# Optimization experiments

Hardware: AMD Instinct MI355X
Metric: run time of the kernel (lower is better)

## Reference

```python
import jax, jax.numpy as jnp
import numpy as np

B, T, C, H = 2, 2048, 1024, 16
D = C // H
EPS = 1e-5
ROPE_BASE = 10000.0


def _rope_tables(t, d, base=ROPE_BASE):
    half = d // 2
    inv_freq = 1.0 / (base ** (jnp.arange(half, dtype=jnp.float32) / half))
    freqs = jnp.arange(t, dtype=jnp.float32)[:, None] * inv_freq[None, :]  # [T, D/2]
    emb = jnp.concatenate([freqs, freqs], axis=-1)  # [T, D]
    return jnp.cos(emb), jnp.sin(emb)


def _rotate_half(x):
    a, b = jnp.split(x, 2, axis=-1)
    return jnp.concatenate([-b, a], axis=-1)


def setup_inputs() -> dict:
    key = jax.random.key(0)
    k0, k1, k2 = jax.random.split(key, 3)
    s = 0.02  # typical init scale
    return {
        "x": jax.random.normal(k0, (B, T, C), jnp.float32),
        "attention_mask": jnp.ones((B, T), jnp.int32),
        "w_qkv": jax.random.normal(k1, (3 * C, C), jnp.float32) * s,
        "b_qkv": jnp.zeros((3 * C,), jnp.float32),
        "w_o": jax.random.normal(k2, (C, C), jnp.float32) * s,
        "b_o": jnp.zeros((C,), jnp.float32),
        "rms_w": jnp.ones((C,), jnp.float32),
    }


def reference(x, attention_mask, w_qkv, b_qkv, w_o, b_o, rms_w):
    b, t, c = x.shape
    h = H
    d = c // h
    # RMSNorm
    xn = x * jax.lax.rsqrt(jnp.mean(x * x, axis=-1, keepdims=True) + EPS) * rms_w
    # fused QKV projection -> [B, T, 3, H, D]
    qkv = (jnp.einsum('btc,oc->bto', xn, w_qkv) + b_qkv).reshape(b, t, 3, h, d)
    q, k, v = qkv[:, :, 0], qkv[:, :, 1], qkv[:, :, 2]
    # RoPE (position_ids = arange(T))
    cos, sin = _rope_tables(t, d)
    cos = cos[None, :, None, :]  # [1, T, 1, D]
    sin = sin[None, :, None, :]
    q = q * cos + _rotate_half(q) * sin
    k = k * cos + _rotate_half(k) * sin
    # causal attention (flash_attn_func semantics: scale 1/sqrt(d), causal)
    scores = jnp.einsum('bqhd,bkhd->bhqk', q, k) / jnp.sqrt(jnp.float32(d))
    causal = jnp.tril(jnp.ones((t, t), dtype=bool))
    scores = jnp.where(causal[None, None], scores, jnp.float32(-1e30))
    attn = jax.nn.softmax(scores, axis=-1)
    out = jnp.einsum('bhqk,bkhd->bqhd', attn, v).reshape(b, t, c)
    return jnp.einsum('btc,oc->bto', out, w_o) + b_o
```

## Files before the change

kernel.cpp:

```cpp
#include <hip/hip_runtime.h>
#include <math.h>

constexpr int Bb = 2;
constexpr int Tt = 2048;
constexpr int Cc = 1024;
constexpr int Hh = 16;
constexpr int M_ROWS = Bb * Tt;
constexpr float EPSV = 1e-5f;

typedef __attribute__((ext_vector_type(4))) float f32x4;
typedef __attribute__((ext_vector_type(8))) __bf16 bf16x8;
using u16 = unsigned short;

union Frag8 {
    u16 u[8];
    unsigned int ui[4];
    uint4 v;
    bf16x8 b;
};

__device__ __forceinline__ u16 f2bf(float f) {
    union { float f; unsigned int u; } c;
    c.f = f;
    unsigned int r = (c.u + 0x7fffu + ((c.u >> 16) & 1u)) >> 16;
    return (u16)r;
}
__device__ __forceinline__ float bf2f(u16 u) {
    union { unsigned int i; float f; } c;
    c.i = ((unsigned int)u) << 16;
    return c.f;
}

__device__ __forceinline__ void gload_lds16(const void* g, void* l) {
    __builtin_amdgcn_global_load_lds(
        (__attribute__((address_space(1))) void*)const_cast<void*>(g),
        (__attribute__((address_space(3))) void*)l, 16, 0, 0);
}

__global__ __launch_bounds__(256) void prep_k(const float* __restrict__ w_qkv,
                                              u16* __restrict__ wqkv_bf,
                                              const float* __restrict__ w_o,
                                              u16* __restrict__ wo_bf,
                                              float* __restrict__ cosT,
                                              float* __restrict__ sinT) {
    int blk = blockIdx.x;
    if (blk < 3072) {
        int i = (blk * 256 + threadIdx.x) * 4;
        float4 v = *(const float4*)&w_qkv[i];
        ushort4 o;
        o.x = f2bf(v.x); o.y = f2bf(v.y); o.z = f2bf(v.z); o.w = f2bf(v.w);
        *(ushort4*)&wqkv_bf[i] = o;
    } else if (blk < 4096) {
        int i = ((blk - 3072) * 256 + threadIdx.x) * 4;
        float4 v = *(const float4*)&w_o[i];
        ushort4 o;
        o.x = f2bf(v.x); o.y = f2bf(v.y); o.z = f2bf(v.z); o.w = f2bf(v.w);
        *(ushort4*)&wo_bf[i] = o;
    } else {
        int lin = (blk - 4096) * 256 + threadIdx.x;
        int tt = lin >> 5, j = lin & 31;
        float inv = exp2f(-(float)j * (log2f(10000.0f) / 32.0f));
        float a = (float)tt * inv;
        cosT[lin] = cosf(a);
        sinT[lin] = sinf(a);
    }
}

__global__ __launch_bounds__(256) void rmsnorm_k(const float* __restrict__ x,
                                                 const float* __restrict__ w,
                                                 u16* __restrict__ xn) {
    int row = blockIdx.x;
    int tid = threadIdx.x;
    const float* xr = x + (size_t)row * Cc;
    float4 v = *(const float4*)&xr[tid * 4];
    float ss = v.x * v.x + v.y * v.y + v.z * v.z + v.w * v.w;
    #pragma unroll
    for (int off = 32; off > 0; off >>= 1) ss += __shfl_down(ss, off);
    __shared__ float ws_[4];
    if ((tid & 63) == 0) ws_[tid >> 6] = ss;
    __syncthreads();
    float tot = ws_[0] + ws_[1] + ws_[2] + ws_[3];
    float r = rsqrtf(tot * (1.0f / (float)Cc) + EPSV);
    float4 wv = *(const float4*)&w[tid * 4];
    ushort4 o;
    o.x = f2bf(v.x * r * wv.x);
    o.y = f2bf(v.y * r * wv.y);
    o.z = f2bf(v.z * r * wv.z);
    o.w = f2bf(v.w * r * wv.w);
    *(ushort4*)&xn[(size_t)row * Cc + tid * 4] = o;
}

template<bool BF16OUT>
__global__ __launch_bounds__(256) void gemm_mfma_k(const u16* __restrict__ A,
                                                   const u16* __restrict__ W,
                                                   const float* __restrict__ bias,
                                                   void* __restrict__ Ov,
                                                   int M, int N, int K) {
    __shared__ __align__(16) u16 As[128 * 64];
    __shared__ __align__(16) u16 Bs[64 * 64];

    const int tid = threadIdx.x;
    const int w = tid >> 6;
    const int l = tid & 63;
    const int wr = w >> 1;
    const int wc = w & 1;
    const int q = l & 15;
    const int g = l >> 4;

    const int m0 = blockIdx.y * 128;
    const int n0 = blockIdx.x * 64;

    const int srow = l >> 3;
    const int cph = l & 7;
    const int cl = cph ^ srow;

    f32x4 acc[4][2];
    #pragma unroll
    for (int i = 0; i < 4; ++i)
        #pragma unroll
        for (int j = 0; j < 2; ++j)
            acc[i][j] = (f32x4){0.f, 0.f, 0.f, 0.f};

    const int nkt = K >> 6;
    for (int kt = 0; kt < nkt; ++kt) {
        const int k0 = kt << 6;
        __syncthreads();
        #pragma unroll
        for (int iss = 0; iss < 4; ++iss) {
            int r = w * 32 + iss * 8 + srow;
            gload_lds16(A + (size_t)(m0 + r) * K + k0 + cl * 8,
                        &As[(w * 32 + iss * 8) * 64]);
        }
        #pragma unroll
        for (int iss = 0; iss < 2; ++iss) {
            int r = w * 16 + iss * 8 + srow;
            gload_lds16(W + (size_t)(n0 + r) * K + k0 + cl * 8,
                        &Bs[(w * 16 + iss * 8) * 64]);
        }
        __syncthreads();

        #pragma unroll
        for (int kk = 0; kk < 2; ++kk) {
            Frag8 af[4], bf[2];
            const int ca = kk * 4 + g;
            #pragma unroll
            for (int i = 0; i < 4; ++i) {
                int ra = wr * 64 + i * 16 + q;
                af[i] = *(const Frag8*)&As[ra * 64 + ((ca ^ (ra & 7)) * 8)];
            }
            #pragma unroll
            for (int j = 0; j < 2; ++j) {
                int rb = wc * 32 + j * 16 + q;
                bf[j] = *(const Frag8*)&Bs[rb * 64 + ((ca ^ (rb & 7)) * 8)];
            }
            #pragma unroll
            for (int i = 0; i < 4; ++i)
                #pragma unroll
                for (int j = 0; j < 2; ++j)
                    acc[i][j] = __builtin_amdgcn_mfma_f32_16x16x32_bf16(
                        af[i].b, bf[j].b, acc[i][j], 0, 0, 0);
        }
    }

    #pragma unroll
    for (int i = 0; i < 4; ++i) {
        int row = m0 + wr * 64 + i * 16 + g * 4;
        #pragma unroll
        for (int j = 0; j < 2; ++j) {
            int col = n0 + wc * 32 + j * 16 + q;
            float bb = bias[col];
            #pragma unroll
            for (int r2 = 0; r2 < 4; ++r2) {
                float val = acc[i][j][r2] + bb;
                if (BF16OUT)
                    ((u16*)Ov)[(size_t)(row + r2) * N + col] = f2bf(val);
                else
                    ((float*)Ov)[(size_t)(row + r2) * N + col] = val;
            }
        }
    }
}

__global__ __launch_bounds__(256) void rope_pack_k(const u16* __restrict__ qkv,
                                                   const float* __restrict__ cosT,
                                                   const float* __restrict__ sinT,
                                                   u16* __restrict__ Qb,
                                                   u16* __restrict__ Kb,
                                                   u16* __restrict__ Vt) {
    const int t0 = blockIdx.x * 64;
    const int h = blockIdx.y, b = blockIdx.z;
    const int t = threadIdx.x;
    const int bh = b * Hh + h;
    __shared__ u16 Vs[64 * 64];
    constexpr float QSC = 0.125f * 1.44269504089f;

    {
        int row = t >> 2, d16 = (t & 3) * 16;
        const u16* vp = qkv + (size_t)(b * Tt + t0 + row) * 3072 + 2048 + h * 64 + d16;
        *(uint4*)&Vs[row * 64 + d16]     = *(const uint4*)vp;
        *(uint4*)&Vs[row * 64 + d16 + 8] = *(const uint4*)(vp + 8);
    }

    {
        int row = t >> 2, d0 = (t & 3) * 8;
        size_t rb = (size_t)(b * Tt + t0 + row) * 3072 + h * 64;
        const u16* qp = qkv + rb;
        const u16* kp = qkv + rb + 1024;
        Frag8 qlo, qhi, klo, khi;
        qlo.v = *(const uint4*)&qp[d0];
        qhi.v = *(const uint4*)&qp[d0 + 32];
        klo.v = *(const uint4*)&kp[d0];
        khi.v = *(const uint4*)&kp[d0 + 32];
        const float* cp = &cosT[(t0 + row) * 32 + d0];
        const float* sp = &sinT[(t0 + row) * 32 + d0];
        float4 c0 = *(const float4*)cp, c1 = *(const float4*)(cp + 4);
        float4 s0 = *(const float4*)sp, s1 = *(const float4*)(sp + 4);
        float cc[8] = {c0.x, c0.y, c0.z, c0.w, c1.x, c1.y, c1.z, c1.w};
        float ss[8] = {s0.x, s0.y, s0.z, s0.w, s1.x, s1.y, s1.z, s1.w};
        Frag8 oql, oqh, okl, okh;
        #pragma unroll
        for (int i = 0; i < 8; ++i) {
            float ql = bf2f(qlo.u[i]), qh = bf2f(qhi.u[i]);
            float kl = bf2f(klo.u[i]), kh = bf2f(khi.u[i]);
            oql.u[i] = f2bf((ql * cc[i] - qh * ss[i]) * QSC);
            oqh.u[i] = f2bf((qh * cc[i] + ql * ss[i]) * QSC);
            okl.u[i] = f2bf(kl * cc[i] - kh * ss[i]);
            okh.u[i] = f2bf(kh * cc[i] + kl * ss[i]);
        }
        u16* qd = Qb + ((size_t)bh * Tt + t0 + row) * 64;
        u16* kd = Kb + ((size_t)bh * Tt + t0 + row) * 64;
        *(uint4*)&qd[d0]      = oql.v;
        *(uint4*)&qd[d0 + 32] = oqh.v;
        *(uint4*)&kd[d0]      = okl.v;
        *(uint4*)&kd[d0 + 32] = okh.v;
    }
    __syncthreads();

    {
        int d = t >> 2, kq = (t & 3) * 16;
        Frag8 a, b2;
        #pragma unroll
        for (int j = 0; j < 16; ++j) {
            int slot = kq + j;
            int key = ((slot >> 5) * 2 + ((slot >> 2) & 1)) * 16
                    + ((slot >> 3) & 3) * 4 + (slot & 3);
            u16 vv = Vs[key * 64 + d];
            if (j < 8) a.u[j] = vv; else b2.u[j - 8] = vv;
        }
        u16* vd = Vt + ((size_t)bh * 64 + d) * Tt + t0 + kq;
        *(uint4*)&vd[0] = a.v;
        *(uint4*)&vd[8] = b2.v;
    }
}

__global__ __launch_bounds__(512) void attn_mfma_k(const u16* __restrict__ Qb,
                                                   const u16* __restrict__ Kb,
                                                   const u16* __restrict__ Vt,
                                                   u16* __restrict__ out) {
    const int i = blockIdx.x;
    const int p = i >> 5;
    const int bh = i & 31;
    const int cH = 31 - p, cL = p;
    const int b = bh >> 4, h = bh & 15;

    const int t = threadIdx.x;
    const int w = t >> 6;
    const int team = w >> 2;
    const int w4 = w & 3;
    const int l = t & 63;
    const int q15 = l & 15;
    const int g2 = l >> 4;

    __shared__ __align__(16) u16 Ks[2][64 * 64];
    __shared__ __align__(16) u16 VTs[2][64 * 64];

    const int cc = team ? cL : cH;

    Frag8 qf[2];
    {
        int qrow = cc * 64 + w4 * 16 + q15;
        const u16* qp = Qb + ((size_t)bh * Tt + qrow) * 64;
        qf[0] = *(const Frag8*)&qp[g2 * 8];
        qf[1] = *(const Frag8*)&qp[32 + g2 * 8];
    }

    Frag8 ones;
    #pragma unroll
    for (int e = 0; e < 8; ++e) ones.u[e] = 0x3F80;

    f32x4 acco[4];
    #pragma unroll
    for (int dg = 0; dg < 4; ++dg) acco[dg] = (f32x4){0.f, 0.f, 0.f, 0.f};
    f32x4 acc_l = (f32x4){0.f, 0.f, 0.f, 0.f};

    const int srow = l >> 3;
    const int cph = l & 7;
    const int xsw = cph ^ srow;
    const int rr = w * 8 + srow;
    const u16* Kbase = Kb + (size_t)bh * Tt * 64;
    const u16* Vbase = Vt + (size_t)bh * 64 * Tt;

    gload_lds16(Kbase + (size_t)rr * 64 + xsw * 8, &Ks[0][(w * 8) * 64]);
    gload_lds16(Vbase + (size_t)rr * Tt + xsw * 8, &VTs[0][(w * 8) * 64]);
    __syncthreads();

    int cur = 0;
    for (int j = 0; j <= cH; ++j) {
        if (j < cH) {
            gload_lds16(Kbase + (size_t)((j + 1) * 64 + rr) * 64 + xsw * 8,
                        &Ks[cur ^ 1][(w * 8) * 64]);
            gload_lds16(Vbase + (size_t)rr * Tt + (j + 1) * 64 + xsw * 8,
                        &VTs[cur ^ 1][(w * 8) * 64]);
        }

        if (!(team == 1 && j > cL)) {
            const u16* Kc = Ks[cur];
            const u16* Vc = VTs[cur];

            f32x4 sacc[4];
            __builtin_amdgcn_s_setprio(1);
            #pragma unroll
            for (int g = 0; g < 4; ++g) {
                sacc[g] = (f32x4){0.f, 0.f, 0.f, 0.f};
                int krow = g * 16 + q15;
                #pragma unroll
                for (int kk = 0; kk < 2; ++kk) {
                    Frag8 kf = *(const Frag8*)&Kc[krow * 64 + (((kk * 4 + g2) ^ (krow & 7)) * 8)];
                    sacc[g] = __builtin_amdgcn_mfma_f32_16x16x32_bf16(
                        kf.b, qf[kk].b, sacc[g], 0, 0, 0);
                }
            }
            __builtin_amdgcn_s_setprio(0);
            if (j == cc) {
                #pragma unroll
                for (int g = 0; g < 4; ++g)
                    #pragma unroll
                    for (int r = 0; r < 4; ++r)
                        if (g * 16 + g2 * 4 + r > w4 * 16 + q15) sacc[g][r] = -1e30f;
            }

            Frag8 pa[2];
            #pragma unroll
            for (int kk = 0; kk < 2; ++kk)
                #pragma unroll
                for (int e = 0; e < 8; ++e)
                    pa[kk].b[e] = (__bf16)exp2f(sacc[2 * kk + (e >> 2)][e & 3]);

            __builtin_amdgcn_s_setprio(1);
            acc_l = __builtin_amdgcn_mfma_f32_16x16x32_bf16(pa[0].b, ones.b, acc_l, 0, 0, 0);
            acc_l = __builtin_amdgcn_mfma_f32_16x16x32_bf16(pa[1].b, ones.b, acc_l, 0, 0, 0);
            #pragma unroll
            for (int dg = 0; dg < 4; ++dg) {
                int vrow = dg * 16 + q15;
                #pragma unroll
                for (int kk = 0; kk < 2; ++kk) {
                    Frag8 vf = *(const Frag8*)&Vc[vrow * 64 + (((kk * 4 + g2) ^ (vrow & 7)) * 8)];
                    acco[dg] = __builtin_amdgcn_mfma_f32_16x16x32_bf16(
                        pa[kk].b, vf.b, acco[dg], 0, 0, 0);
                }
            }
            __builtin_amdgcn_s_setprio(0);
        }

        if (j < cH) __syncthreads();
        cur ^= 1;
    }

    float lr[4];
    #pragma unroll
    for (int r = 0; r < 4; ++r) lr[r] = 1.f / acc_l[r];
    const int qbase = cc * 64 + w4 * 16;
    #pragma unroll
    for (int dg = 0; dg < 4; ++dg)
        #pragma unroll
        for (int r = 0; r < 4; ++r)
            out[((size_t)(b * Tt + qbase + g2 * 4 + r)) * Cc + h * 64 + dg * 16 + q15] =
                f2bf(acco[dg][r] * lr[r]);
}

extern "C" void kernel_launch(void* const* d_in, const int* in_sizes, int n_in,
                              void* d_out, int out_size, void* d_ws, size_t ws_size,
                              hipStream_t stream) {
    const float* x      = (const float*)d_in[0];
    const float* w_qkv  = (const float*)d_in[2];
    const float* b_qkv  = (const float*)d_in[3];
    const float* w_o    = (const float*)d_in[4];
    const float* b_o    = (const float*)d_in[5];
    const float* rms_w  = (const float*)d_in[6];
    float* out = (float*)d_out;

    char* ws = (char*)d_ws;
    u16*   xn_bf   = (u16*)ws;
    u16*   Kb      = (u16*)(ws + (size_t)(8 << 20));
    u16*   Vt      = (u16*)(ws + (size_t)(16 << 20));
    u16*   Qb      = (u16*)(ws + (size_t)(24 << 20));
    u16*   qkvb    = (u16*)(ws + (size_t)(32 << 20));
    u16*   wqkv_bf = (u16*)(ws + (size_t)(56 << 20));
    u16*   wo_bf   = (u16*)(ws + (size_t)(62 << 20));
    float* cosT    = (float*)(ws + (size_t)(64 << 20));
    float* sinT    = (float*)(ws + (size_t)(64 << 20) + (1 << 18));
    u16*   attn_bf = xn_bf;

    prep_k<<<dim3(4352), dim3(256), 0, stream>>>(w_qkv, wqkv_bf, w_o, wo_bf,
                                                 cosT, sinT);
    rmsnorm_k<<<dim3(M_ROWS), dim3(256), 0, stream>>>(x, rms_w, xn_bf);
    gemm_mfma_k<true><<<dim3(3 * Cc / 64, M_ROWS / 128), dim3(256), 0, stream>>>(
        xn_bf, wqkv_bf, b_qkv, qkvb, M_ROWS, 3 * Cc, Cc);
    rope_pack_k<<<dim3(Tt / 64, Hh, Bb), dim3(256), 0, stream>>>(
        qkvb, cosT, sinT, Qb, Kb, Vt);
    attn_mfma_k<<<dim3(512), dim3(512), 0, stream>>>(Qb, Kb, Vt, attn_bf);
    gemm_mfma_k<false><<<dim3(Cc / 64, M_ROWS / 128), dim3(256), 0, stream>>>(
        attn_bf, wo_bf, b_o, out, M_ROWS, Cc, Cc);
}
```

Measured before the change: 117.5 us.

## Split attention KV range across two teams per query block; fuse rmsnorm into prep

The attention kernel no longer pairs a heavy and a light query chunk per block. Each block now handles a single 64-row query chunk and splits its causal KV tiles between two 4-wave teams, then merges the partial sums through LDS, with twice as many blocks launched. Since there is no running max, the two partials can simply be added. The double-buffered prefetch is replaced by a single buffer per team with two barriers per iteration, so load latency is now exposed. Separately, rmsnorm is folded into the prep kernel to save one launch.

```diff
diff --git a/kernel.cpp b/kernel.cpp
--- a/kernel.cpp
+++ b/kernel.cpp
@@ -42,52 +42,51 @@
                                               const float* __restrict__ w_o,
                                               u16* __restrict__ wo_bf,
                                               float* __restrict__ cosT,
-                                              float* __restrict__ sinT) {
+                                              float* __restrict__ sinT,
+                                              const float* __restrict__ x,
+                                              const float* __restrict__ rms_w,
+                                              u16* __restrict__ xn) {
+    __shared__ float ws_[4];
     int blk = blockIdx.x;
+    int tid = threadIdx.x;
     if (blk < 3072) {
-        int i = (blk * 256 + threadIdx.x) * 4;
+        int i = (blk * 256 + tid) * 4;
         float4 v = *(const float4*)&w_qkv[i];
         ushort4 o;
         o.x = f2bf(v.x); o.y = f2bf(v.y); o.z = f2bf(v.z); o.w = f2bf(v.w);
         *(ushort4*)&wqkv_bf[i] = o;
     } else if (blk < 4096) {
-        int i = ((blk - 3072) * 256 + threadIdx.x) * 4;
+        int i = ((blk - 3072) * 256 + tid) * 4;
         float4 v = *(const float4*)&w_o[i];
         ushort4 o;
         o.x = f2bf(v.x); o.y = f2bf(v.y); o.z = f2bf(v.z); o.w = f2bf(v.w);
         *(ushort4*)&wo_bf[i] = o;
-    } else {
-        int lin = (blk - 4096) * 256 + threadIdx.x;
+    } else if (blk < 4352) {
+        int lin = (blk - 4096) * 256 + tid;
         int tt = lin >> 5, j = lin & 31;
         float inv = exp2f(-(float)j * (log2f(10000.0f) / 32.0f));
         float a = (float)tt * inv;
         cosT[lin] = cosf(a);
         sinT[lin] = sinf(a);
-    }
-}
-
-__global__ __launch_bounds__(256) void rmsnorm_k(const float* __restrict__ x,
-                                                 const float* __restrict__ w,
-                                                 u16* __restrict__ xn) {
-    int row = blockIdx.x;
-    int tid = threadIdx.x;
-    const float* xr = x + (size_t)row * Cc;
-    float4 v = *(const float4*)&xr[tid * 4];
-    float ss = v.x * v.x + v.y * v.y + v.z * v.z + v.w * v.w;
-    #pragma unroll
-    for (int off = 32; off > 0; off >>= 1) ss += __shfl_down(ss, off);
-    __shared__ float ws_[4];
-    if ((tid & 63) == 0) ws_[tid >> 6] = ss;
-    __syncthreads();
-    float tot = ws_[0] + ws_[1] + ws_[2] + ws_[3];
-    float r = rsqrtf(tot * (1.0f / (float)Cc) + EPSV);
-    float4 wv = *(const float4*)&w[tid * 4];
-    ushort4 o;
-    o.x = f2bf(v.x * r * wv.x);
-    o.y = f2bf(v.y * r * wv.y);
-    o.z = f2bf(v.z * r * wv.z);
-    o.w = f2bf(v.w * r * wv.w);
-    *(ushort4*)&xn[(size_t)row * Cc + tid * 4] = o;
+    } else {
+        int row = blk - 4352;
+        const float* xr = x + (size_t)row * Cc;
+        float4 v = *(const float4*)&xr[tid * 4];
+        float ss = v.x * v.x + v.y * v.y + v.z * v.z + v.w * v.w;
+        #pragma unroll
+        for (int off = 32; off > 0; off >>= 1) ss += __shfl_down(ss, off);
+        if ((tid & 63) == 0) ws_[tid >> 6] = ss;
+        __syncthreads();
+        float tot = ws_[0] + ws_[1] + ws_[2] + ws_[3];
+        float r = rsqrtf(tot * (1.0f / (float)Cc) + EPSV);
+        float4 wv = *(const float4*)&rms_w[tid * 4];
+        ushort4 o;
+        o.x = f2bf(v.x * r * wv.x);
+        o.y = f2bf(v.y * r * wv.y);
+        o.z = f2bf(v.z * r * wv.z);
+        o.w = f2bf(v.w * r * wv.w);
+        *(ushort4*)&xn[(size_t)row * Cc + tid * 4] = o;
+    }
 }
 
 template<bool BF16OUT>
@@ -258,9 +257,9 @@
                                                    const u16* __restrict__ Vt,
                                                    u16* __restrict__ out) {
     const int i = blockIdx.x;
-    const int p = i >> 5;
-    const int bh = i & 31;
-    const int cH = 31 - p, cL = p;
+    int c, bh;
+    if (i < 512) { c = 31 - (i >> 5); bh = i & 31; }
+    else         { int k = i - 512; c = k >> 5; bh = k & 31; }
     const int b = bh >> 4, h = bh & 15;
 
     const int t = threadIdx.x;
@@ -271,14 +270,19 @@
     const int q15 = l & 15;
     const int g2 = l >> 4;
 
-    __shared__ __align__(16) u16 Ks[2][64 * 64];
-    __shared__ __align__(16) u16 VTs[2][64 * 64];
-
-    const int cc = team ? cL : cH;
+    __shared__ __align__(16) char lds[32768];
+    u16* Ksm = (u16*)(lds + team * 8192);
+    u16* Vsm = (u16*)(lds + 16384 + team * 8192);
+    float* red = (float*)lds;
+
+    const int nj = c + 1;
+    const int h0 = (nj + 1) >> 1;
+    const int myn = team ? (nj - h0) : h0;
+    const int jbase = team ? h0 : 0;
 
     Frag8 qf[2];
     {
-        int qrow = cc * 64 + w4 * 16 + q15;
+        int qrow = c * 64 + w4 * 16 + q15;
         const u16* qp = Qb + ((size_t)bh * Tt + qrow) * 64;
         qf[0] = *(const Frag8*)&qp[g2 * 8];
         qf[1] = *(const Frag8*)&qp[32 + g2 * 8];
@@ -296,27 +300,24 @@
     const int srow = l >> 3;
     const int cph = l & 7;
     const int xsw = cph ^ srow;
-    const int rr = w * 8 + srow;
     const u16* Kbase = Kb + (size_t)bh * Tt * 64;
     const u16* Vbase = Vt + (size_t)bh * 64 * Tt;
 
-    gload_lds16(Kbase + (size_t)rr * 64 + xsw * 8, &Ks[0][(w * 8) * 64]);
-    gload_lds16(Vbase + (size_t)rr * Tt + xsw * 8, &VTs[0][(w * 8) * 64]);
-    __syncthreads();
-
-    int cur = 0;
-    for (int j = 0; j <= cH; ++j) {
-        if (j < cH) {
-            gload_lds16(Kbase + (size_t)((j + 1) * 64 + rr) * 64 + xsw * 8,
-                        &Ks[cur ^ 1][(w * 8) * 64]);
-            gload_lds16(Vbase + (size_t)rr * Tt + (j + 1) * 64 + xsw * 8,
-                        &VTs[cur ^ 1][(w * 8) * 64]);
-        }
-
-        if (!(team == 1 && j > cL)) {
-            const u16* Kc = Ks[cur];
-            const u16* Vc = VTs[cur];
-
+    for (int it = 0; it < h0; ++it) {
+        __syncthreads();
+        const int j = jbase + it;
+        if (it < myn) {
+            #pragma unroll
+            for (int iss = 0; iss < 2; ++iss) {
+                int rr = w4 * 16 + iss * 8 + srow;
+                gload_lds16(Kbase + (size_t)(j * 64 + rr) * 64 + xsw * 8,
+                            &Ksm[(w4 * 16 + iss * 8) * 64]);
+                gload_lds16(Vbase + (size_t)rr * Tt + j * 64 + xsw * 8,
+                            &Vsm[(w4 * 16 + iss * 8) * 64]);
+            }
+        }
+        __syncthreads();
+        if (it < myn) {
             f32x4 sacc[4];
             __builtin_amdgcn_s_setprio(1);
             #pragma unroll
@@ -325,13 +326,13 @@
                 int krow = g * 16 + q15;
                 #pragma unroll
                 for (int kk = 0; kk < 2; ++kk) {
-                    Frag8 kf = *(const Frag8*)&Kc[krow * 64 + (((kk * 4 + g2) ^ (krow & 7)) * 8)];
+                    Frag8 kf = *(const Frag8*)&Ksm[krow * 64 + (((kk * 4 + g2) ^ (krow & 7)) * 8)];
                     sacc[g] = __builtin_amdgcn_mfma_f32_16x16x32_bf16(
                         kf.b, qf[kk].b, sacc[g], 0, 0, 0);
                 }
             }
             __builtin_amdgcn_s_setprio(0);
-            if (j == cc) {
+            if (j == c) {
                 #pragma unroll
                 for (int g = 0; g < 4; ++g)
                     #pragma unroll
@@ -354,28 +355,45 @@
                 int vrow = dg * 16 + q15;
                 #pragma unroll
                 for (int kk = 0; kk < 2; ++kk) {
-                    Frag8 vf = *(const Frag8*)&Vc[vrow * 64 + (((kk * 4 + g2) ^ (vrow & 7)) * 8)];
+                    Frag8 vf = *(const Frag8*)&Vsm[vrow * 64 + (((kk * 4 + g2) ^ (vrow & 7)) * 8)];
                     acco[dg] = __builtin_amdgcn_mfma_f32_16x16x32_bf16(
                         pa[kk].b, vf.b, acco[dg], 0, 0, 0);
                 }
             }
             __builtin_amdgcn_s_setprio(0);
         }
-
-        if (j < cH) __syncthreads();
-        cur ^= 1;
-    }
-
-    float lr[4];
-    #pragma unroll
-    for (int r = 0; r < 4; ++r) lr[r] = 1.f / acc_l[r];
-    const int qbase = cc * 64 + w4 * 16;
-    #pragma unroll
-    for (int dg = 0; dg < 4; ++dg)
-        #pragma unroll
-        for (int r = 0; r < 4; ++r)
-            out[((size_t)(b * Tt + qbase + g2 * 4 + r)) * Cc + h * 64 + dg * 16 + q15] =
-                f2bf(acco[dg][r] * lr[r]);
+    }
+
+    __syncthreads();
+    const int slot = (w4 * 64 + l) * 20;
+    if (team == 1) {
+        #pragma unroll
+        for (int dg = 0; dg < 4; ++dg)
+            #pragma unroll
+            for (int r = 0; r < 4; ++r) red[slot + dg * 4 + r] = acco[dg][r];
+        #pragma unroll
+        for (int r = 0; r < 4; ++r) red[slot + 16 + r] = acc_l[r];
+    }
+    __syncthreads();
+    if (team == 0) {
+        #pragma unroll
+        for (int dg = 0; dg < 4; ++dg)
+            #pragma unroll
+            for (int r = 0; r < 4; ++r) acco[dg][r] += red[slot + dg * 4 + r];
+        #pragma unroll
+        for (int r = 0; r < 4; ++r) acc_l[r] += red[slot + 16 + r];
+
+        float lr[4];
+        #pragma unroll
+        for (int r = 0; r < 4; ++r) lr[r] = 1.f / acc_l[r];
+        const int qbase = c * 64 + w4 * 16;
+        #pragma unroll
+        for (int dg = 0; dg < 4; ++dg)
+            #pragma unroll
+            for (int r = 0; r < 4; ++r)
+                out[((size_t)(b * Tt + qbase + g2 * 4 + r)) * Cc + h * 64 + dg * 16 + q15] =
+                    f2bf(acco[dg][r] * lr[r]);
+    }
 }
 
 extern "C" void kernel_launch(void* const* d_in, const int* in_sizes, int n_in,
@@ -401,14 +419,13 @@
     float* sinT    = (float*)(ws + (size_t)(64 << 20) + (1 << 18));
     u16*   attn_bf = xn_bf;
 
-    prep_k<<<dim3(4352), dim3(256), 0, stream>>>(w_qkv, wqkv_bf, w_o, wo_bf,
-                                                 cosT, sinT);
-    rmsnorm_k<<<dim3(M_ROWS), dim3(256), 0, stream>>>(x, rms_w, xn_bf);
+    prep_k<<<dim3(8448), dim3(256), 0, stream>>>(w_qkv, wqkv_bf, w_o, wo_bf,
+                                                 cosT, sinT, x, rms_w, xn_bf);
     gemm_mfma_k<true><<<dim3(3 * Cc / 64, M_ROWS / 128), dim3(256), 0, stream>>>(
         xn_bf, wqkv_bf, b_qkv, qkvb, M_ROWS, 3 * Cc, Cc);
     rope_pack_k<<<dim3(Tt / 64, Hh, Bb), dim3(256), 0, stream>>>(
         qkvb, cosT, sinT, Qb, Kb, Vt);
-    attn_mfma_k<<<dim3(512), dim3(512), 0, stream>>>(Qb, Kb, Vt, attn_bf);
+    attn_mfma_k<<<dim3(1024), dim3(512), 0, stream>>>(Qb, Kb, Vt, attn_bf);
     gemm_mfma_k<false><<<dim3(Cc / 64, M_ROWS / 128), dim3(256), 0, stream>>>(
         attn_bf, wo_bf, b_o, out, M_ROWS, Cc, Cc);
 }
```

Measured after the change: 113.7 us, median of 2. 1.03x faster.
